# Performance work log

Hardware: AMD Instinct MI355X
Metric: run time of the kernel (lower is better)

Reference implementation:

```python
import jax, jax.numpy as jnp
import numpy as np

N_NODES = 100000
N_EDGES = 3200000
IN_DIM = 128
EMB = 32
NUM_GRAPHS = 256


def setup_inputs() -> dict:
    key = jax.random.key(0)
    ks = jax.random.split(key, 7)
    x = jax.random.normal(ks[0], (N_NODES, IN_DIM), dtype=jnp.float32)
    edge_index = jax.random.randint(ks[1], (2, N_EDGES), 0, N_NODES, dtype=jnp.int64)
    batch_index = jnp.sort(jax.random.randint(ks[2], (N_NODES,), 0, NUM_GRAPHS, dtype=jnp.int64))
    W1 = jax.random.normal(ks[3], (IN_DIM, EMB), dtype=jnp.float32) * (1.0 / np.sqrt(IN_DIM))
    b1 = jax.random.normal(ks[4], (EMB,), dtype=jnp.float32) * 0.01
    Wout = jax.random.normal(ks[5], (2 * EMB, 1), dtype=jnp.float32) * (1.0 / np.sqrt(2 * EMB))
    bout = jax.random.normal(ks[6], (1,), dtype=jnp.float32) * 0.01
    return {"x": x, "edge_index": edge_index, "batch_index": batch_index,
            "W1": W1, "b1": b1, "Wout": Wout, "bout": bout}


def gcn_conv(x, edge_index, W, b):
    """PyG GCNConv: add self-loops, symmetric deg^-1/2 normalization, XW, scatter-add, +bias."""
    N = x.shape[0]
    xw = x @ W  # [N, out]
    src, dst = edge_index[0], edge_index[1]
    # degree includes self-loop (+1)
    deg = jax.ops.segment_sum(jnp.ones(src.shape[0], dtype=xw.dtype), dst, num_segments=N) + 1.0
    dinv = jax.lax.rsqrt(deg)  # deg >= 1 so safe
    norm = dinv[src] * dinv[dst]  # [E]
    msg = xw[src] * norm[:, None]  # [E, out]
    agg = jax.ops.segment_sum(msg, dst, num_segments=N)
    # self-loop contribution: dinv[i]^2 * xw[i]
    agg = agg + xw * (dinv * dinv)[:, None]
    return agg + b


def reference(x, edge_index, batch_index, W1, b1, Wout, bout):
    h = gcn_conv(x, edge_index, W1, b1)           # [N, EMB]
    h = jnp.tanh(h)
    sums = jax.ops.segment_sum(h, batch_index, num_segments=NUM_GRAPHS)   # global_add_pool
    counts = jax.ops.segment_sum(jnp.ones((h.shape[0],), dtype=h.dtype), batch_index, num_segments=NUM_GRAPHS)
    means = sums / jnp.maximum(counts, 1.0)[:, None]                       # global_mean_pool
    pooled = jnp.concatenate([sums, means], axis=1)  # [G, 2*EMB]
    return pooled @ Wout + bout                      # [G, 1]
```

## Files before the change

kernel.cpp:

```cpp
#include <hip/hip_runtime.h>
#include <hip/hip_fp16.h>

#define N_NODES    100000
#define N_EDGES    3200000
#define IN_DIM     128
#define EMB        32
#define NUM_GRAPHS 256

#define FB         1024
#define NODES_PB   128
#define NBUCKETS   782
#define F1_EPB     20000
#define F1_BLOCKS  160
#define H_EPB      20000
#define H_BLOCKS   160
#define XW_BLOCKS  1563
#define CAP        5632

typedef _Float16 half8 __attribute__((ext_vector_type(8)));
typedef float floatx4 __attribute__((ext_vector_type(4)));

__global__ __launch_bounds__(512) void k_hist1(const int* __restrict__ ei,
                                               int* __restrict__ chist) {
    __shared__ int h[FB];
    int t = threadIdx.x;
    for (int i = t; i < FB; i += 512) h[i] = 0;
    __syncthreads();
    int e0 = blockIdx.x * H_EPB;
    int e1 = e0 + H_EPB; if (e1 > N_EDGES) e1 = N_EDGES;
    for (int e = e0 + t; e < e1; e += 512)
        atomicAdd(&h[ei[N_EDGES + e] >> 7], 1);
    __syncthreads();
    for (int i = t; i < FB; i += 512)
        if (h[i]) atomicAdd(&chist[i], h[i]);
}

__global__ __launch_bounds__(512) void k_aux(const int* __restrict__ chist,
                                             int* __restrict__ cbase,
                                             int* __restrict__ gcursor,
                                             const int* __restrict__ batch,
                                             float* __restrict__ sums,
                                             float* __restrict__ counts) {
    int t = threadIdx.x;
    if (blockIdx.x == 0) {
        __shared__ int ts[512];
        int v0 = chist[2 * t], v1 = chist[2 * t + 1];
        int tot = v0 + v1;
        ts[t] = tot;
        __syncthreads();
        for (int off = 1; off < 512; off <<= 1) {
            int u = (t >= off) ? ts[t - off] : 0;
            __syncthreads();
            ts[t] += u;
            __syncthreads();
        }
        int base = ts[t] - tot;
        cbase[2 * t] = base;          gcursor[2 * t] = base;
        cbase[2 * t + 1] = base + v0; gcursor[2 * t + 1] = base + v0;
        if (t == 511) cbase[FB] = ts[511];
    } else {
        for (int i = t; i < NUM_GRAPHS * EMB; i += 512) sums[i] = 0.f;
        if (t < NUM_GRAPHS) {
            int lo = 0, hi = N_NODES;
            while (lo < hi) { int mid = (lo + hi) >> 1; if (batch[mid] < t) lo = mid + 1; else hi = mid; }
            int a = lo;
            lo = 0; hi = N_NODES;
            int g1 = t + 1;
            while (lo < hi) { int mid = (lo + hi) >> 1; if (batch[mid] < g1) lo = mid + 1; else hi = mid; }
            counts[t] = (float)(lo - a);
        }
    }
}

__global__ __launch_bounds__(512) void k_fill1(const int* __restrict__ ei,
                                               int* __restrict__ gcursor,
                                               unsigned int* __restrict__ recs) {
    __shared__ int hist[FB];
    __shared__ int base[FB];
    __shared__ int lcur[FB];
    int t = threadIdx.x;
    for (int i = t; i < FB; i += 512) { hist[i] = 0; lcur[i] = 0; }
    __syncthreads();
    int e0 = blockIdx.x * F1_EPB;
    int e1 = e0 + F1_EPB; if (e1 > N_EDGES) e1 = N_EDGES;
    for (int e = e0 + t; e < e1; e += 512)
        atomicAdd(&hist[ei[N_EDGES + e] >> 7], 1);
    __syncthreads();
    for (int i = t; i < FB; i += 512)
        if (hist[i]) base[i] = atomicAdd(&gcursor[i], hist[i]);
    __syncthreads();
    for (int e = e0 + t; e < e1; e += 512) {
        int s = ei[e];
        int d = ei[N_EDGES + e];
        int b = d >> 7;
        int pos = base[b] + atomicAdd(&lcur[b], 1);
        recs[pos] = ((unsigned int)(d & 127) << 24) | (unsigned int)s;
    }
}

__global__ __launch_bounds__(512) void k_fill2(const unsigned int* __restrict__ recs,
                                               const int* __restrict__ cbase,
                                               int* __restrict__ edge_src,
                                               int* __restrict__ rowstart,
                                               float* __restrict__ dinv) {
    __shared__ unsigned int lbuf[CAP];
    __shared__ int h2[NODES_PB], cur2[NODES_PB], sc[NODES_PB];
    int t = threadIdx.x, b = blockIdx.x;
    if (t < NODES_PB) h2[t] = 0;
    __syncthreads();
    int seg0 = cbase[b];
    int cnt = cbase[b + 1] - seg0;
    for (int j = t; j < cnt; j += 512) {
        unsigned int r = recs[seg0 + j];
        if (j < CAP) lbuf[j] = r;
        atomicAdd(&h2[r >> 24], 1);
    }
    __syncthreads();
    int v = 0;
    if (t < NODES_PB) { v = h2[t]; sc[t] = v; }
    __syncthreads();
    for (int off = 1; off < NODES_PB; off <<= 1) {
        int u = 0;
        if (t < NODES_PB && t >= off) u = sc[t - off];
        __syncthreads();
        if (t < NODES_PB) sc[t] += u;
        __syncthreads();
    }
    int node0 = b << 7;
    if (t < NODES_PB) {
        int excl = sc[t] - v;
        cur2[t] = excl;
        int node = node0 + t;
        if (node < N_NODES) {
            rowstart[node] = seg0 + excl;
            dinv[node] = rsqrtf((float)v + 1.0f);
        }
    }
    if (b == 0 && t == 0) rowstart[N_NODES] = N_EDGES;
    __syncthreads();
    for (int j = t; j < cnt; j += 512) {
        unsigned int r = (j < CAP) ? lbuf[j] : recs[seg0 + j];
        int p = atomicAdd(&cur2[r >> 24], 1);
        edge_src[seg0 + p] = (int)(r & 0x00FFFFFF);
    }
}

__global__ __launch_bounds__(256) void k_xw(const float* __restrict__ x,
                                            const float* __restrict__ W1,
                                            const float* __restrict__ dinv,
                                            __half* __restrict__ xwh) {
    __shared__ _Float16 Wh[IN_DIM * (EMB + 1)];
    for (int i = threadIdx.x; i < IN_DIM * EMB; i += 256)
        Wh[(i >> 5) * (EMB + 1) + (i & 31)] = (_Float16)W1[i];
    __syncthreads();
    int wave = threadIdx.x >> 6;
    int lane = threadIdx.x & 63;
    int m = lane & 15, quad = lane >> 4;
    int row0 = (blockIdx.x * 4 + wave) * 16;
    if (row0 >= N_NODES) return;
    half8 bfrag[2][4];
#pragma unroll
    for (int nt = 0; nt < 2; ++nt)
#pragma unroll
        for (int ks = 0; ks < 4; ++ks)
#pragma unroll
            for (int j = 0; j < 8; ++j)
                bfrag[nt][ks][j] = Wh[(ks * 32 + quad * 8 + j) * (EMB + 1) + nt * 16 + m];
    const float* xr = x + (size_t)(row0 + m) * IN_DIM + quad * 8;
    floatx4 c0 = {0.f, 0.f, 0.f, 0.f}, c1 = {0.f, 0.f, 0.f, 0.f};
#pragma unroll
    for (int ks = 0; ks < 4; ++ks) {
        float4 a0 = *(const float4*)(xr + ks * 32);
        float4 a1 = *(const float4*)(xr + ks * 32 + 4);
        half8 af;
        af[0] = (_Float16)a0.x; af[1] = (_Float16)a0.y;
        af[2] = (_Float16)a0.z; af[3] = (_Float16)a0.w;
        af[4] = (_Float16)a1.x; af[5] = (_Float16)a1.y;
        af[6] = (_Float16)a1.z; af[7] = (_Float16)a1.w;
        c0 = __builtin_amdgcn_mfma_f32_16x16x32_f16(af, bfrag[0][ks], c0, 0, 0, 0);
        c1 = __builtin_amdgcn_mfma_f32_16x16x32_f16(af, bfrag[1][ks], c1, 0, 0, 0);
    }
#pragma unroll
    for (int r = 0; r < 4; ++r) {
        int ro = row0 + quad * 4 + r;
        float di = dinv[ro];
        xwh[(size_t)ro * EMB + m]      = __float2half(c0[r] * di);
        xwh[(size_t)ro * EMB + 16 + m] = __float2half(c1[r] * di);
    }
}

template<int K>
__device__ __forceinline__ void gstep(const int* __restrict__ es,
                                      const __half2* __restrict__ rows,
                                      int cc, int e, float& a0, float& a1) {
    int s[K];
    float2 f[K];
#pragma unroll
    for (int k = 0; k < K; ++k) s[k] = es[e + k];
#pragma unroll
    for (int k = 0; k < K; ++k) f[k] = __half22float2(rows[s[k] * 16 + cc]);
#pragma unroll
    for (int k = 0; k < K; ++k) { a0 += f[k].x; a1 += f[k].y; }
}

__global__ __launch_bounds__(256) void k_gather(const __half* __restrict__ xws,
                                                const float* __restrict__ dinv,
                                                const int* __restrict__ rowstart,
                                                const int* __restrict__ edge_src,
                                                const int* __restrict__ batch,
                                                const float* __restrict__ b1,
                                                float* __restrict__ sums) {
    const __half2* rows = (const __half2*)xws;
    int grp = threadIdx.x >> 4;
    int cc  = threadIdx.x & 15;
    int i = blockIdx.x * 16 + grp;
    float di = dinv[i];
    int e0 = rowstart[i], e1 = rowstart[i + 1];
    float a0 = 0.f, a1 = 0.f;
    int e = e0;
    for (; e + 16 <= e1; e += 16) gstep<16>(edge_src, rows, cc, e, a0, a1);
    if (e + 8 <= e1) { gstep<8>(edge_src, rows, cc, e, a0, a1); e += 8; }
    if (e + 4 <= e1) { gstep<4>(edge_src, rows, cc, e, a0, a1); e += 4; }
    if (e + 2 <= e1) { gstep<2>(edge_src, rows, cc, e, a0, a1); e += 2; }
    if (e < e1)      { gstep<1>(edge_src, rows, cc, e, a0, a1); }
    float2 fs = __half22float2(rows[i * 16 + cc]);
    float2 bb = *(const float2*)(b1 + 2 * cc);
    float h0 = tanhf((a0 + fs.x) * di + bb.x);
    float h1 = tanhf((a1 + fs.y) * di + bb.y);

    __shared__ float hs[16][EMB];
    __shared__ int gb[16];
    *(float2*)&hs[grp][2 * cc] = make_float2(h0, h1);
    if (cc == 0) gb[grp] = batch[i];
    __syncthreads();
    if (threadIdx.x < 32) {
        int col = threadIdx.x;
        int rr = 0;
        while (rr < 16) {
            int g0 = gb[rr];
            float a = hs[rr][col];
            int r2 = rr + 1;
            while (r2 < 16 && gb[r2] == g0) { a += hs[r2][col]; ++r2; }
            atomicAdd(&sums[g0 * EMB + col], a);
            rr = r2;
        }
    }
}

__global__ __launch_bounds__(64) void k_out(const float* __restrict__ sums,
                                            const float* __restrict__ counts,
                                            const float* __restrict__ Wout,
                                            const float* __restrict__ bout,
                                            float* __restrict__ out) {
    int g = blockIdx.x * 64 + threadIdx.x;
    if (g >= NUM_GRAPHS) return;
    float inv = 1.0f / fmaxf(counts[g], 1.0f);
    float acc = bout[0];
#pragma unroll
    for (int c = 0; c < EMB; ++c) {
        float s = sums[g * EMB + c];
        acc += s * Wout[c] + s * inv * Wout[EMB + c];
    }
    out[g] = acc;
}

extern "C" void kernel_launch(void* const* d_in, const int* in_sizes, int n_in,
                              void* d_out, int out_size, void* d_ws, size_t ws_size,
                              hipStream_t stream) {
    const float* x     = (const float*)d_in[0];
    const int*   ei    = (const int*)d_in[1];
    const int*   batch = (const int*)d_in[2];
    const float* W1    = (const float*)d_in[3];
    const float* b1    = (const float*)d_in[4];
    const float* Wout  = (const float*)d_in[5];
    const float* bout  = (const float*)d_in[6];
    float* out = (float*)d_out;

    char* ws = (char*)d_ws;
    __half* xwh        = (__half*)ws;       ws += (size_t)N_NODES * EMB * sizeof(__half);
    unsigned int* recs = (unsigned int*)ws; ws += (size_t)N_EDGES * sizeof(int);
    int*   edge_src    = (int*)ws;          ws += (size_t)N_EDGES * sizeof(int);
    int*   rowstart    = (int*)ws;          ws += (size_t)(N_NODES + 4) * sizeof(int);
    float* dinv        = (float*)ws;        ws += (size_t)N_NODES * sizeof(float);
    int*   chist       = (int*)ws;          ws += FB * sizeof(int);
    int*   cbase       = (int*)ws;          ws += (FB + 2) * sizeof(int);
    int*   gcursor     = (int*)ws;          ws += FB * sizeof(int);
    float* sums        = (float*)ws;        ws += (size_t)NUM_GRAPHS * EMB * sizeof(float);
    float* counts      = (float*)ws;

    hipMemsetAsync(chist, 0, FB * sizeof(int), stream);

    k_hist1 <<<H_BLOCKS, 512, 0, stream>>>(ei, chist);
    k_aux   <<<2, 512, 0, stream>>>(chist, cbase, gcursor, batch, sums, counts);
    k_fill1 <<<F1_BLOCKS, 512, 0, stream>>>(ei, gcursor, recs);
    k_fill2 <<<NBUCKETS, 512, 0, stream>>>(recs, cbase, edge_src, rowstart, dinv);
    k_xw    <<<XW_BLOCKS, 256, 0, stream>>>(x, W1, dinv, xwh);
    k_gather<<<N_NODES / 16, 256, 0, stream>>>(xwh, dinv, rowstart, edge_src, batch, b1, sums);
    k_out   <<<(NUM_GRAPHS + 63) / 64, 64, 0, stream>>>(sums, counts, Wout, bout, out);
}
```

Before: 227.8 us.

## Replace global-atomic bucket scatter with per-block histograms and two-level prefix scan

Coarse bucketing of edges by destination now builds a per-block histogram table (512 blocks) and computes exact per-block bucket offsets with a chunked two-level scan. The fill pass then only needs shared-memory atomics seeded from these offsets. The separate global histogram, its memset, the global cursor atomics, and the second histogram pass inside fill are all removed. More, smaller blocks raise parallelism, at the cost of extra launches and scratch traffic for the 512x1024 histogram table, which reuses the edge_src buffer before it is written.

```diff
diff --git a/kernel.cpp b/kernel.cpp
--- a/kernel.cpp
+++ b/kernel.cpp
@@ -10,90 +10,103 @@
 #define FB         1024
 #define NODES_PB   128
 #define NBUCKETS   782
-#define F1_EPB     20000
-#define F1_BLOCKS  160
-#define H_EPB      20000
-#define H_BLOCKS   160
+#define FB_B       512
+#define FB_EPB     6250
+#define NCHUNK     16
+#define CHROWS     32
 #define XW_BLOCKS  1563
 #define CAP        5632
 
 typedef _Float16 half8 __attribute__((ext_vector_type(8)));
 typedef float floatx4 __attribute__((ext_vector_type(4)));
 
-__global__ __launch_bounds__(512) void k_hist1(const int* __restrict__ ei,
-                                               int* __restrict__ chist) {
+__global__ __launch_bounds__(512) void k_hist(const int* __restrict__ ei,
+                                              int* __restrict__ bhist) {
     __shared__ int h[FB];
     int t = threadIdx.x;
     for (int i = t; i < FB; i += 512) h[i] = 0;
     __syncthreads();
-    int e0 = blockIdx.x * H_EPB;
-    int e1 = e0 + H_EPB; if (e1 > N_EDGES) e1 = N_EDGES;
-    for (int e = e0 + t; e < e1; e += 512)
+    int e0 = blockIdx.x * FB_EPB;
+    for (int e = e0 + t; e < e0 + FB_EPB; e += 512)
         atomicAdd(&h[ei[N_EDGES + e] >> 7], 1);
     __syncthreads();
-    for (int i = t; i < FB; i += 512)
-        if (h[i]) atomicAdd(&chist[i], h[i]);
-}
-
-__global__ __launch_bounds__(512) void k_aux(const int* __restrict__ chist,
-                                             int* __restrict__ cbase,
-                                             int* __restrict__ gcursor,
-                                             const int* __restrict__ batch,
-                                             float* __restrict__ sums,
-                                             float* __restrict__ counts) {
+    for (int i = t; i < FB; i += 512) bhist[blockIdx.x * FB + i] = h[i];
+}
+
+__global__ __launch_bounds__(512) void k_part(const int* __restrict__ bhist,
+                                              int* __restrict__ part) {
+    int j = blockIdx.x, t = threadIdx.x;
+    int row0 = j * CHROWS;
+    for (int b = t; b < FB; b += 512) {
+        int acc = 0;
+#pragma unroll 8
+        for (int i = 0; i < CHROWS; ++i) acc += bhist[(row0 + i) * FB + b];
+        part[j * FB + b] = acc;
+    }
+}
+
+__global__ __launch_bounds__(1024) void k_mid(const int* __restrict__ bhist,
+                                              const int* __restrict__ part,
+                                              int* __restrict__ bbase,
+                                              int* __restrict__ cbase) {
+    __shared__ int ts[FB];
+    int b = threadIdx.x;
+    int j = blockIdx.x;
+    int tot = 0;
+#pragma unroll
+    for (int k = 0; k < NCHUNK; ++k) tot += part[k * FB + b];
+    ts[b] = tot;
+    __syncthreads();
+    for (int off = 1; off < FB; off <<= 1) {
+        int u = (b >= off) ? ts[b - off] : 0;
+        __syncthreads();
+        ts[b] += u;
+        __syncthreads();
+    }
+    int cb = ts[b] - tot;
+    if (j == 0) {
+        cbase[b] = cb;
+        if (b == 0) cbase[FB] = N_EDGES;
+    }
+    int run = cb;
+    for (int k = 0; k < j; ++k) run += part[k * FB + b];
+    int row0 = j * CHROWS;
+    for (int i = 0; i < CHROWS; ++i) {
+        int h = bhist[(row0 + i) * FB + b];
+        bbase[(row0 + i) * FB + b] = run;
+        run += h;
+    }
+}
+
+__global__ __launch_bounds__(512) void k_aux2(const int* __restrict__ batch,
+                                              float* __restrict__ sums,
+                                              float* __restrict__ counts) {
     int t = threadIdx.x;
-    if (blockIdx.x == 0) {
-        __shared__ int ts[512];
-        int v0 = chist[2 * t], v1 = chist[2 * t + 1];
-        int tot = v0 + v1;
-        ts[t] = tot;
-        __syncthreads();
-        for (int off = 1; off < 512; off <<= 1) {
-            int u = (t >= off) ? ts[t - off] : 0;
-            __syncthreads();
-            ts[t] += u;
-            __syncthreads();
-        }
-        int base = ts[t] - tot;
-        cbase[2 * t] = base;          gcursor[2 * t] = base;
-        cbase[2 * t + 1] = base + v0; gcursor[2 * t + 1] = base + v0;
-        if (t == 511) cbase[FB] = ts[511];
-    } else {
-        for (int i = t; i < NUM_GRAPHS * EMB; i += 512) sums[i] = 0.f;
-        if (t < NUM_GRAPHS) {
-            int lo = 0, hi = N_NODES;
-            while (lo < hi) { int mid = (lo + hi) >> 1; if (batch[mid] < t) lo = mid + 1; else hi = mid; }
-            int a = lo;
-            lo = 0; hi = N_NODES;
-            int g1 = t + 1;
-            while (lo < hi) { int mid = (lo + hi) >> 1; if (batch[mid] < g1) lo = mid + 1; else hi = mid; }
-            counts[t] = (float)(lo - a);
-        }
-    }
-}
-
-__global__ __launch_bounds__(512) void k_fill1(const int* __restrict__ ei,
-                                               int* __restrict__ gcursor,
-                                               unsigned int* __restrict__ recs) {
-    __shared__ int hist[FB];
-    __shared__ int base[FB];
+    for (int i = t; i < NUM_GRAPHS * EMB; i += 512) sums[i] = 0.f;
+    if (t < NUM_GRAPHS) {
+        int lo = 0, hi = N_NODES;
+        while (lo < hi) { int mid = (lo + hi) >> 1; if (batch[mid] < t) lo = mid + 1; else hi = mid; }
+        int a = lo;
+        lo = 0; hi = N_NODES;
+        int g1 = t + 1;
+        while (lo < hi) { int mid = (lo + hi) >> 1; if (batch[mid] < g1) lo = mid + 1; else hi = mid; }
+        counts[t] = (float)(lo - a);
+    }
+}
+
+__global__ __launch_bounds__(512) void k_fill(const int* __restrict__ ei,
+                                              const int* __restrict__ bbase,
+                                              unsigned int* __restrict__ recs) {
     __shared__ int lcur[FB];
     int t = threadIdx.x;
-    for (int i = t; i < FB; i += 512) { hist[i] = 0; lcur[i] = 0; }
-    __syncthreads();
-    int e0 = blockIdx.x * F1_EPB;
-    int e1 = e0 + F1_EPB; if (e1 > N_EDGES) e1 = N_EDGES;
-    for (int e = e0 + t; e < e1; e += 512)
-        atomicAdd(&hist[ei[N_EDGES + e] >> 7], 1);
-    __syncthreads();
-    for (int i = t; i < FB; i += 512)
-        if (hist[i]) base[i] = atomicAdd(&gcursor[i], hist[i]);
-    __syncthreads();
-    for (int e = e0 + t; e < e1; e += 512) {
+    for (int i = t; i < FB; i += 512) lcur[i] = bbase[blockIdx.x * FB + i];
+    __syncthreads();
+    int e0 = blockIdx.x * FB_EPB;
+    for (int e = e0 + t; e < e0 + FB_EPB; e += 512) {
         int s = ei[e];
         int d = ei[N_EDGES + e];
         int b = d >> 7;
-        int pos = base[b] + atomicAdd(&lcur[b], 1);
+        int pos = atomicAdd(&lcur[b], 1);
         recs[pos] = ((unsigned int)(d & 127) << 24) | (unsigned int)s;
     }
 }
@@ -282,17 +295,19 @@
     int*   edge_src    = (int*)ws;          ws += (size_t)N_EDGES * sizeof(int);
     int*   rowstart    = (int*)ws;          ws += (size_t)(N_NODES + 4) * sizeof(int);
     float* dinv        = (float*)ws;        ws += (size_t)N_NODES * sizeof(float);
-    int*   chist       = (int*)ws;          ws += FB * sizeof(int);
     int*   cbase       = (int*)ws;          ws += (FB + 2) * sizeof(int);
-    int*   gcursor     = (int*)ws;          ws += FB * sizeof(int);
     float* sums        = (float*)ws;        ws += (size_t)NUM_GRAPHS * EMB * sizeof(float);
     float* counts      = (float*)ws;
 
-    hipMemsetAsync(chist, 0, FB * sizeof(int), stream);
-
-    k_hist1 <<<H_BLOCKS, 512, 0, stream>>>(ei, chist);
-    k_aux   <<<2, 512, 0, stream>>>(chist, cbase, gcursor, batch, sums, counts);
-    k_fill1 <<<F1_BLOCKS, 512, 0, stream>>>(ei, gcursor, recs);
+    int* bhist = edge_src;
+    int* part  = edge_src + (size_t)FB_B * FB;
+    int* bbase = part + (size_t)NCHUNK * FB;
+
+    k_aux2  <<<1, 512, 0, stream>>>(batch, sums, counts);
+    k_hist  <<<FB_B, 512, 0, stream>>>(ei, bhist);
+    k_part  <<<NCHUNK, 512, 0, stream>>>(bhist, part);
+    k_mid   <<<NCHUNK, 1024, 0, stream>>>(bhist, part, bbase, cbase);
+    k_fill  <<<FB_B, 512, 0, stream>>>(ei, bbase, recs);
     k_fill2 <<<NBUCKETS, 512, 0, stream>>>(recs, cbase, edge_src, rowstart, dinv);
     k_xw    <<<XW_BLOCKS, 256, 0, stream>>>(x, W1, dinv, xwh);
     k_gather<<<N_NODES / 16, 256, 0, stream>>>(xwh, dinv, rowstart, edge_src, batch, b1, sums);
```

New measurement: 227.4 us. About the same (-0.1%).
